# Optimization experiments

Measured on AMD Instinct MI355X. Metric: run time of the kernel, lower is better.

## Reference

```python
import jax, jax.numpy as jnp
import numpy as np

GROUP_SIZE = 128
HIDDEN = 2048
INTER = 5632
TOKENS = 8192
_SHIFTS = jnp.arange(8, dtype=jnp.uint32) * 4  # 4-bit nibbles, 8 per int32


def _pack_rows(nib):
    # nib: [in, out] int values in [0,16); pack 8 consecutive rows into one int32
    r, c = nib.shape
    n = nib.reshape(r // 8, 8, c).astype(jnp.uint32)
    packed = jnp.sum(n << _SHIFTS[None, :, None], axis=1, dtype=jnp.uint32)
    return jax.lax.bitcast_convert_type(packed, jnp.int32)  # [in//8, out]


def _pack_cols(nib):
    # nib: [groups, out]; pack 8 consecutive cols into one int32
    g, o = nib.shape
    n = nib.reshape(g, o // 8, 8).astype(jnp.uint32)
    packed = jnp.sum(n << _SHIFTS[None, None, :], axis=-1, dtype=jnp.uint32)
    return jax.lax.bitcast_convert_type(packed, jnp.int32)  # [groups, out//8]


def _dequant(qweight, qzeros, scales, group_size=GROUP_SIZE):
    # GPTQ int4 dequant: w = (q - (z + 1)) * scale, per group of `group_size` input rows
    in_packed, out = qweight.shape
    in_dim = in_packed * 8
    groups = scales.shape[0]
    sh = jnp.arange(8, dtype=jnp.int32) * 4
    q = (qweight[:, None, :] >> sh[None, :, None]) & 0xF       # [in//8, 8, out]
    q = q.reshape(in_dim, out)
    z = (qzeros[:, :, None] >> sh[None, None, :]) & 0xF        # [groups, out//8, 8]
    z = z.reshape(groups, out)
    gidx = jnp.arange(in_dim) // group_size                    # [in]
    w = (q - (z[gidx] + 1)).astype(scales.dtype) * scales[gidx]
    return w  # [in, out]


def setup_inputs() -> dict:
    key = jax.random.key(0)
    ks = jax.random.split(key, 10)
    x = jax.random.normal(ks[0], (TOKENS, HIDDEN), dtype=jnp.float32)

    def make(kq, kz, ksc, in_dim, out_dim):
        qn = jax.random.randint(kq, (in_dim, out_dim), 0, 16, dtype=jnp.int32)
        zn = jax.random.randint(kz, (in_dim // GROUP_SIZE, out_dim), 0, 16, dtype=jnp.int32)
        sc = jax.random.uniform(ksc, (in_dim // GROUP_SIZE, out_dim), jnp.float32, 1e-3, 2e-2)
        return _pack_rows(qn), _pack_cols(zn), sc

    gq, gz, gs = make(ks[1], ks[2], ks[3], HIDDEN, INTER)
    uq, uz, us = make(ks[4], ks[5], ks[6], HIDDEN, INTER)
    dq, dz, ds = make(ks[7], ks[8], ks[9], INTER, HIDDEN)
    return {
        "x": x,
        "gate_qweight": gq, "gate_qzeros": gz, "gate_scales": gs,
        "up_qweight": uq, "up_qzeros": uz, "up_scales": us,
        "down_qweight": dq, "down_qzeros": dz, "down_scales": ds,
    }


def reference(x, gate_qweight, gate_qzeros, gate_scales,
              up_qweight, up_qzeros, up_scales,
              down_qweight, down_qzeros, down_scales):
    wg = _dequant(gate_qweight, gate_qzeros, gate_scales)  # [H, I]
    wu = _dequant(up_qweight, up_qzeros, up_scales)        # [H, I]
    wd = _dequant(down_qweight, down_qzeros, down_scales)  # [I, H]
    # fused_gate_up: silu(x @ Wg) * (x @ Wu)
    h = jax.nn.silu(x @ wg) * (x @ wu)                     # [T, I]
    return h @ wd                                          # [T, H]
```

## Files before the change

### kernel.cpp

```cpp
#include <hip/hip_runtime.h>

#define TOKENS 8192
#define HIDDEN 2048
#define INTER  5632

typedef _Float16 f16x8 __attribute__((ext_vector_type(8)));
typedef float    f32x4 __attribute__((ext_vector_type(4)));

__device__ __forceinline__ void async_copy16(const void* g, void* l) {
  __builtin_amdgcn_global_load_lds(
      (const __attribute__((address_space(1))) unsigned int*)g,
      (__attribute__((address_space(3))) unsigned int*)l, 16, 0, 0);
}

#define BAR   __builtin_amdgcn_s_barrier()
#define SB0   __builtin_amdgcn_sched_barrier(0)
#define LGKM0 do { asm volatile("s_waitcnt lgkmcnt(0)" ::: "memory"); SB0; } while (0)
#define WAITVM(n) asm volatile("s_waitcnt vmcnt(" #n ")" ::: "memory")
#define PRIO(x) __builtin_amdgcn_s_setprio(x)


__global__ __launch_bounds__(256)
void k_convert_x(const float* __restrict__ x, _Float16* __restrict__ xs) {
  __shared__ float lt[64 * 33];
  const int kb0  = blockIdx.x;
  const int mt32 = blockIdx.y;
  const int t    = threadIdx.x;

  const int m_l  = t >> 3;
  const int k4a  = t & 7;
  const float* row = x + (size_t)(mt32 * 32 + m_l) * HIDDEN + kb0 * 64;
#pragma unroll
  for (int h = 0; h < 2; ++h) {
    const int k4 = k4a + h * 8;
    const float4 f = *(const float4*)(row + k4 * 4);
    lt[(k4 * 4 + 0) * 33 + m_l] = f.x;
    lt[(k4 * 4 + 1) * 33 + m_l] = f.y;
    lt[(k4 * 4 + 2) * 33 + m_l] = f.z;
    lt[(k4 * 4 + 3) * 33 + m_l] = f.w;
  }
  __syncthreads();

  const int kb_l = t >> 5;
  const int m_o  = t & 31;
  f16x8 v;
#pragma unroll
  for (int j = 0; j < 8; ++j)
    v[j] = (_Float16)lt[(kb_l * 8 + j) * 33 + m_o];
  const int kb   = kb0 * 8 + kb_l;
  const int mt128 = mt32 >> 2;
  const int m128  = (mt32 & 3) * 32 + m_o;
  *(f16x8*)(xs + ((size_t)(mt128 * 256 + kb) * 128 + m128) * 8) = v;
}

__global__ void k_dequant(const unsigned int* __restrict__ qw,
                          const unsigned int* __restrict__ qz,
                          const float* __restrict__ sc,
                          _Float16* __restrict__ out, int N, int N8) {
  const int n  = blockIdx.x * 256 + threadIdx.x;
  const int k8 = blockIdx.y;
  const int g  = k8 >> 4;
  unsigned int q  = qw[(size_t)k8 * N + n];
  unsigned int zw = qz[(size_t)g * N8 + (n >> 3)];
  int   z1 = (int)((zw >> ((n & 7) * 4)) & 0xFu) + 1;
  float s  = sc[(size_t)g * N + n];
  f16x8 w;
#pragma unroll
  for (int j = 0; j < 8; ++j)
    w[j] = (_Float16)((float)((int)((q >> (4 * j)) & 0xFu) - z1) * s);
  *(f16x8*)(out + ((size_t)k8 * N + n) * 8) = w;
}

__global__ __launch_bounds__(256, 2)
void k_gemm_gateup(const _Float16* __restrict__ xs,
                   const _Float16* __restrict__ wg,
                   const _Float16* __restrict__ wu,
                   _Float16* __restrict__ hs) {
  __shared__ _Float16 lds[3 * 8192];
  _Float16* Al  = lds;
  _Float16* Bgl = lds + 8192;
  _Float16* Bul = lds + 16384;
  const int nt = blockIdx.x, mt = blockIdx.y;
  const int tid = threadIdx.x;
  const int wave = tid >> 6, lane = tid & 63;
  const int wm = wave >> 1, wn = wave & 1;
  const int row16 = lane >> 4, col = lane & 15;
  const int slot = wave * 4;

  const _Float16* gA = xs + (size_t)mt * 256 * 1024;

  int afo[4], bfo[4];
#pragma unroll
  for (int i = 0; i < 4; ++i) {
    afo[i] = (row16 * 128 + wm * 64 + i * 16 + col) * 8;
    bfo[i] = (row16 * 128 + wn * 64 + i * 16 + col) * 8;
  }

  const f32x4 zero = {0.f, 0.f, 0.f, 0.f};
  f32x4 accg[4][4], accu[4][4];
#pragma unroll
  for (int i = 0; i < 4; ++i)
#pragma unroll
    for (int j = 0; j < 4; ++j) { accg[i][j] = zero; accu[i][j] = zero; }

  for (int kit = 0; kit < HIDDEN / 64; ++kit) {
    __syncthreads();
#pragma unroll
    for (int q = 0; q < 4; ++q) {
      const int c = (slot + q) * 64 + lane;
      async_copy16(gA + (size_t)kit * 8192 + (size_t)c * 8,
                   (char*)Al + (size_t)(slot + q) * 1024);
      const int kbl = c >> 7, cc = c & 127;
      const size_t bo = ((size_t)(kit * 8 + kbl) * INTER + nt * 128 + cc) * 8;
      async_copy16(wg + bo, (char*)Bgl + (size_t)(slot + q) * 1024);
      async_copy16(wu + bo, (char*)Bul + (size_t)(slot + q) * 1024);
    }
    __syncthreads();
#pragma unroll
    for (int ks = 0; ks < 2; ++ks) {
      const int kadd = ks * 4096;
      f16x8 af[4], bg[4], bu[4];
#pragma unroll
      for (int i = 0; i < 4; ++i) {
        af[i] = *(const f16x8*)(Al  + kadd + afo[i]);
        bg[i] = *(const f16x8*)(Bgl + kadd + bfo[i]);
        bu[i] = *(const f16x8*)(Bul + kadd + bfo[i]);
      }
#pragma unroll
      for (int mi = 0; mi < 4; ++mi)
#pragma unroll
        for (int ni = 0; ni < 4; ++ni) {
          accg[mi][ni] = __builtin_amdgcn_mfma_f32_16x16x32_f16(af[mi], bg[ni], accg[mi][ni], 0, 0, 0);
          accu[mi][ni] = __builtin_amdgcn_mfma_f32_16x16x32_f16(af[mi], bu[ni], accu[mi][ni], 0, 0, 0);
        }
    }
  }
#pragma unroll
  for (int mi = 0; mi < 4; ++mi)
#pragma unroll
    for (int ni = 0; ni < 4; ++ni) {
      const int kg = nt * 128 + wn * 64 + ni * 16 + col;
      const size_t base = (size_t)(mt * (INTER / 8) + (kg >> 3)) * 1024 + (kg & 7);
#pragma unroll
      for (int r = 0; r < 4; ++r) {
        float g = accg[mi][ni][r], u = accu[mi][ni][r];
        float h = g / (1.f + __expf(-g)) * u;
        const int ml = wm * 64 + mi * 16 + row16 * 4 + r;
        hs[base + (size_t)ml * 8] = (_Float16)h;
      }
    }
}

__global__ __launch_bounds__(512, 1)
void k_gemm_down(const _Float16* __restrict__ hs,
                 const _Float16* __restrict__ wd,
                 float* __restrict__ out) {
  extern __shared__ _Float16 lds[];
  _Float16* A0 = lds;
  _Float16* A1 = lds + 16384;
  _Float16* B0 = lds + 32768;
  _Float16* B1 = lds + 49152;

  const int bid  = blockIdx.x;
  const int wgid = (bid & 7) * 32 + (bid >> 3);
  const int nt = wgid >> 5, mt = wgid & 31;

  const int tid  = threadIdx.x;
  const int wave = tid >> 6, lane = tid & 63;
  const int wm = wave >> 2, wn = wave & 3;
  const int row16 = lane >> 4, col = lane & 15;

  int afo[8], bfo[4];
#pragma unroll
  for (int i = 0; i < 8; ++i)
    afo[i] = wm * 8192 + row16 * 1024 + (i * 16 + col) * 8;
#pragma unroll
  for (int i = 0; i < 4; ++i)
    bfo[i] = row16 * 2048 + (wn * 64 + i * 16 + col) * 8;

  const f32x4 zero = {0.f, 0.f, 0.f, 0.f};
  f32x4 acc[8][4];
#pragma unroll
  for (int i = 0; i < 8; ++i)
#pragma unroll
    for (int j = 0; j < 4; ++j) acc[i][j] = zero;

  f16x8 af[4][2], bf[4][2];

#define DN_LOAD_A(AP, mh) \
  _Pragma("unroll") for (int mi_ = 0; mi_ < 4; ++mi_) \
  _Pragma("unroll") for (int ks_ = 0; ks_ < 2; ++ks_) \
    af[mi_][ks_] = *(const f16x8*)((AP) + afo[(mh) * 4 + mi_] + ks_ * 4096);

#define DN_LOAD_B(BP, nh) \
  _Pragma("unroll") for (int ni_ = 0; ni_ < 2; ++ni_) \
  _Pragma("unroll") for (int ks_ = 0; ks_ < 2; ++ks_) \
    bf[(nh) * 2 + ni_][ks_] = *(const f16x8*)((BP) + bfo[(nh) * 2 + ni_] + ks_ * 8192);

#define DN_MFMA(mh, nh) \
  _Pragma("unroll") for (int mi_ = 0; mi_ < 4; ++mi_) \
  _Pragma("unroll") for (int ni_ = 0; ni_ < 2; ++ni_) \
  _Pragma("unroll") for (int ks_ = 0; ks_ < 2; ++ks_) \
    acc[(mh) * 4 + mi_][(nh) * 2 + ni_] = __builtin_amdgcn_mfma_f32_16x16x32_f16( \
        af[mi_][ks_], bf[(nh) * 2 + ni_][ks_], acc[(mh) * 4 + mi_][(nh) * 2 + ni_], 0, 0, 0);

#define DN_STAGE_A(AP, kt) do { const int kt_ = (kt); \
  _Pragma("unroll") for (int q_ = 0; q_ < 4; ++q_) { \
    const int i_ = q_ * 512 + tid; \
    async_copy16(hs + (size_t)(((2 * mt + (i_ >> 10)) * 704 + kt_ * 8 + ((i_ >> 7) & 7)) * 128 + (i_ & 127)) * 8, \
                 (char*)(AP) + q_ * 8192 + wave * 1024); } } while (0)

#define DN_STAGE_B(BP, kt) do { const int kt_ = (kt); \
  _Pragma("unroll") for (int q_ = 0; q_ < 4; ++q_) { \
    const int i_ = q_ * 512 + tid; \
    async_copy16(wd + (size_t)((kt_ * 8 + (i_ >> 8)) * HIDDEN + nt * 256 + (i_ & 255)) * 8, \
                 (char*)(BP) + q_ * 8192 + wave * 1024); } } while (0)

  DN_STAGE_B(B0, 0); DN_STAGE_A(A0, 0);
  DN_STAGE_B(B1, 1); DN_STAGE_A(A1, 1);
  WAITVM(8);
  BAR; SB0;

  for (int t2 = 0; t2 < 44; ++t2) {
    const int e2 = (2 * t2 + 2 < 88) ? 2 * t2 + 2 : 87;
    const int o2 = (2 * t2 + 3 < 88) ? 2 * t2 + 3 : 87;
    DN_LOAD_A(A0, 0); DN_LOAD_B(B0, 0);
    BAR; LGKM0; PRIO(1); DN_MFMA(0, 0); PRIO(0); BAR; SB0;
    DN_LOAD_B(B0, 1);
    BAR; LGKM0; PRIO(1); DN_MFMA(0, 1); PRIO(0); BAR; SB0;
    DN_LOAD_A(A0, 1); DN_STAGE_B(B0, e2);
    BAR; LGKM0; PRIO(1); DN_MFMA(1, 0); PRIO(0); BAR; SB0;
    DN_STAGE_A(A0, e2);
    BAR; LGKM0; PRIO(1); DN_MFMA(1, 1); PRIO(0); WAITVM(8); BAR; SB0;
    DN_LOAD_A(A1, 0); DN_LOAD_B(B1, 0);
    BAR; LGKM0; PRIO(1); DN_MFMA(0, 0); PRIO(0); BAR; SB0;
    DN_LOAD_B(B1, 1);
    BAR; LGKM0; PRIO(1); DN_MFMA(0, 1); PRIO(0); BAR; SB0;
    DN_LOAD_A(A1, 1); DN_STAGE_B(B1, o2);
    BAR; LGKM0; PRIO(1); DN_MFMA(1, 0); PRIO(0); BAR; SB0;
    DN_STAGE_A(A1, o2);
    BAR; LGKM0; PRIO(1); DN_MFMA(1, 1); PRIO(0); WAITVM(8); BAR; SB0;
  }
  WAITVM(0);

#pragma unroll
  for (int mi = 0; mi < 8; ++mi)
#pragma unroll
    for (int ni = 0; ni < 4; ++ni) {
      const int n = nt * 256 + wn * 64 + ni * 16 + col;
#pragma unroll
      for (int r = 0; r < 4; ++r) {
        const int m = mt * 256 + wm * 128 + mi * 16 + row16 * 4 + r;
        out[(size_t)m * HIDDEN + n] = acc[mi][ni][r];
      }
    }
#undef DN_LOAD_A
#undef DN_LOAD_B
#undef DN_MFMA
#undef DN_STAGE_A
#undef DN_STAGE_B
}

extern "C" void kernel_launch(void* const* d_in, const int* in_sizes, int n_in,
                              void* d_out, int out_size, void* d_ws, size_t ws_size,
                              hipStream_t stream) {
  (void)in_sizes; (void)n_in; (void)out_size; (void)ws_size;
  const float*        x  = (const float*)d_in[0];
  const unsigned int* gq = (const unsigned int*)d_in[1];
  const unsigned int* gz = (const unsigned int*)d_in[2];
  const float*        gs = (const float*)d_in[3];
  const unsigned int* uq = (const unsigned int*)d_in[4];
  const unsigned int* uz = (const unsigned int*)d_in[5];
  const float*        us = (const float*)d_in[6];
  const unsigned int* dq = (const unsigned int*)d_in[7];
  const unsigned int* dz = (const unsigned int*)d_in[8];
  const float*        ds = (const float*)d_in[9];
  float* out = (float*)d_out;

  char* ws = (char*)d_ws;
  _Float16* xs  = (_Float16*)ws;
  _Float16* wgd = (_Float16*)(ws + (size_t)TOKENS * HIDDEN * 2);
  _Float16* wud = wgd + (size_t)HIDDEN * INTER;
  _Float16* wdd = wud + (size_t)HIDDEN * INTER;
  _Float16* hs  = wdd + (size_t)INTER * HIDDEN;

  static bool attr_set = false;
  if (!attr_set) {
    hipFuncSetAttribute((const void*)k_gemm_down,
                        hipFuncAttributeMaxDynamicSharedMemorySize, 131072);
    attr_set = true;
  }

  k_convert_x<<<dim3(HIDDEN / 64, TOKENS / 32), 256, 0, stream>>>(x, xs);
  k_dequant<<<dim3(INTER / 256, HIDDEN / 8), 256, 0, stream>>>(gq, gz, gs, wgd, INTER, INTER / 8);
  k_dequant<<<dim3(INTER / 256, HIDDEN / 8), 256, 0, stream>>>(uq, uz, us, wud, INTER, INTER / 8);
  k_dequant<<<dim3(HIDDEN / 256, INTER / 8), 256, 0, stream>>>(dq, dz, ds, wdd, HIDDEN, HIDDEN / 8);
  k_gemm_gateup<<<dim3(INTER / 128, TOKENS / 128), 256, 0, stream>>>(xs, wgd, wud, hs);
  k_gemm_down<<<dim3(256), 512, 131072, stream>>>(hs, wdd, out);
}
```

Before: 661.3 us.

## Fuse int4 gate/up dequantization into gate-up GEMM using fp16 magic-number trick

Removes the two separate dequant kernels for the gate and up weights. The gate-up GEMM now loads packed int4 words straight from global memory into registers and dequantizes them in-register with the 0x6400 fp16 bias trick and packed half2 subtract/multiply. The x conversion permutes the K order within each group of 8 to match the interleaved nibble layout. This cuts the fp16 weight write and read traffic and two launches, but it adds ALU work and un-staged global loads inside the MFMA loop, and scales are rounded to fp16.

```diff
diff --git a/kernel.cpp b/kernel.cpp
--- a/kernel.cpp
+++ b/kernel.cpp
@@ -5,6 +5,7 @@
 #define INTER  5632
 
 typedef _Float16 f16x8 __attribute__((ext_vector_type(8)));
+typedef _Float16 f16x2 __attribute__((ext_vector_type(2)));
 typedef float    f32x4 __attribute__((ext_vector_type(4)));
 
 __device__ __forceinline__ void async_copy16(const void* g, void* l) {
@@ -18,6 +19,18 @@
 #define LGKM0 do { asm volatile("s_waitcnt lgkmcnt(0)" ::: "memory"); SB0; } while (0)
 #define WAITVM(n) asm volatile("s_waitcnt vmcnt(" #n ")" ::: "memory")
 #define PRIO(x) __builtin_amdgcn_s_setprio(x)
+
+__device__ __forceinline__ f16x8 dq8(unsigned int q, f16x2 s2, f16x2 c2) {
+  union { unsigned int u[4]; f16x8 v; } r;
+#pragma unroll
+  for (int j = 0; j < 4; ++j) {
+    const unsigned int t = ((q >> (4 * j)) & 0x000F000Fu) | 0x64006400u;
+    f16x2 h = __builtin_bit_cast(f16x2, t);
+    h = (h - c2) * s2;
+    r.u[j] = __builtin_bit_cast(unsigned int, h);
+  }
+  return r.v;
+}
 
 
 __global__ __launch_bounds__(256)
@@ -43,10 +56,11 @@
 
   const int kb_l = t >> 5;
   const int m_o  = t & 31;
+  const int P[8] = {0, 4, 1, 5, 2, 6, 3, 7};
   f16x8 v;
 #pragma unroll
   for (int j = 0; j < 8; ++j)
-    v[j] = (_Float16)lt[(kb_l * 8 + j) * 33 + m_o];
+    v[j] = (_Float16)lt[(kb_l * 8 + P[j]) * 33 + m_o];
   const int kb   = kb0 * 8 + kb_l;
   const int mt128 = mt32 >> 2;
   const int m128  = (mt32 & 3) * 32 + m_o;
@@ -73,13 +87,14 @@
 
 __global__ __launch_bounds__(256, 2)
 void k_gemm_gateup(const _Float16* __restrict__ xs,
-                   const _Float16* __restrict__ wg,
-                   const _Float16* __restrict__ wu,
+                   const unsigned int* __restrict__ gq,
+                   const unsigned int* __restrict__ gz,
+                   const float* __restrict__ gs,
+                   const unsigned int* __restrict__ uq,
+                   const unsigned int* __restrict__ uz,
+                   const float* __restrict__ us,
                    _Float16* __restrict__ hs) {
-  __shared__ _Float16 lds[3 * 8192];
-  _Float16* Al  = lds;
-  _Float16* Bgl = lds + 8192;
-  _Float16* Bul = lds + 16384;
+  __shared__ _Float16 Al[8192];
   const int nt = blockIdx.x, mt = blockIdx.y;
   const int tid = threadIdx.x;
   const int wave = tid >> 6, lane = tid & 63;
@@ -89,11 +104,11 @@
 
   const _Float16* gA = xs + (size_t)mt * 256 * 1024;
 
-  int afo[4], bfo[4];
+  int afo[4], ncol[4];
 #pragma unroll
   for (int i = 0; i < 4; ++i) {
-    afo[i] = (row16 * 128 + wm * 64 + i * 16 + col) * 8;
-    bfo[i] = (row16 * 128 + wn * 64 + i * 16 + col) * 8;
+    afo[i]  = (row16 * 128 + wm * 64 + i * 16 + col) * 8;
+    ncol[i] = nt * 128 + wn * 64 + i * 16 + col;
   }
 
   const f32x4 zero = {0.f, 0.f, 0.f, 0.f};
@@ -103,28 +118,59 @@
 #pragma unroll
     for (int j = 0; j < 4; ++j) { accg[i][j] = zero; accu[i][j] = zero; }
 
+  f16x2 sg2[4], cg2[4], su2[4], cu2[4];
+
   for (int kit = 0; kit < HIDDEN / 64; ++kit) {
+    if ((kit & 1) == 0) {
+      const int g = kit >> 1;
+#pragma unroll
+      for (int ni = 0; ni < 4; ++ni) {
+        const int n = ncol[ni];
+        const float        sgf = gs[(size_t)g * INTER + n];
+        const float        suf = us[(size_t)g * INTER + n];
+        const unsigned int zgw = gz[(size_t)g * (INTER / 8) + (n >> 3)];
+        const unsigned int zuw = uz[(size_t)g * (INTER / 8) + (n >> 3)];
+        const int z1g = (int)((zgw >> ((n & 7) * 4)) & 0xFu) + 1;
+        const int z1u = (int)((zuw >> ((n & 7) * 4)) & 0xFu) + 1;
+        const _Float16 shg = (_Float16)sgf, shu = (_Float16)suf;
+        const _Float16 chg = (_Float16)(float)(1024 + z1g);
+        const _Float16 chu = (_Float16)(float)(1024 + z1u);
+        sg2[ni] = (f16x2){shg, shg}; cg2[ni] = (f16x2){chg, chg};
+        su2[ni] = (f16x2){shu, shu}; cu2[ni] = (f16x2){chu, chu};
+      }
+    }
+
+    unsigned int bqg[2][4], bqu[2][4];
+#pragma unroll
+    for (int ks = 0; ks < 2; ++ks) {
+      const size_t ro = (size_t)((kit * 8 + ks * 4 + row16)) * INTER;
+#pragma unroll
+      for (int ni = 0; ni < 4; ++ni) {
+        bqg[ks][ni] = gq[ro + ncol[ni]];
+        bqu[ks][ni] = uq[ro + ncol[ni]];
+      }
+    }
+
     __syncthreads();
 #pragma unroll
     for (int q = 0; q < 4; ++q) {
       const int c = (slot + q) * 64 + lane;
       async_copy16(gA + (size_t)kit * 8192 + (size_t)c * 8,
                    (char*)Al + (size_t)(slot + q) * 1024);
-      const int kbl = c >> 7, cc = c & 127;
-      const size_t bo = ((size_t)(kit * 8 + kbl) * INTER + nt * 128 + cc) * 8;
-      async_copy16(wg + bo, (char*)Bgl + (size_t)(slot + q) * 1024);
-      async_copy16(wu + bo, (char*)Bul + (size_t)(slot + q) * 1024);
     }
     __syncthreads();
+
 #pragma unroll
     for (int ks = 0; ks < 2; ++ks) {
       const int kadd = ks * 4096;
       f16x8 af[4], bg[4], bu[4];
 #pragma unroll
-      for (int i = 0; i < 4; ++i) {
-        af[i] = *(const f16x8*)(Al  + kadd + afo[i]);
-        bg[i] = *(const f16x8*)(Bgl + kadd + bfo[i]);
-        bu[i] = *(const f16x8*)(Bul + kadd + bfo[i]);
+      for (int i = 0; i < 4; ++i)
+        af[i] = *(const f16x8*)(Al + kadd + afo[i]);
+#pragma unroll
+      for (int ni = 0; ni < 4; ++ni) {
+        bg[ni] = dq8(bqg[ks][ni], sg2[ni], cg2[ni]);
+        bu[ni] = dq8(bqu[ks][ni], su2[ni], cu2[ni]);
       }
 #pragma unroll
       for (int mi = 0; mi < 4; ++mi)
@@ -139,7 +185,7 @@
   for (int mi = 0; mi < 4; ++mi)
 #pragma unroll
     for (int ni = 0; ni < 4; ++ni) {
-      const int kg = nt * 128 + wn * 64 + ni * 16 + col;
+      const int kg = ncol[ni];
       const size_t base = (size_t)(mt * (INTER / 8) + (kg >> 3)) * 1024 + (kg & 7);
 #pragma unroll
       for (int r = 0; r < 4; ++r) {
@@ -279,9 +325,7 @@
 
   char* ws = (char*)d_ws;
   _Float16* xs  = (_Float16*)ws;
-  _Float16* wgd = (_Float16*)(ws + (size_t)TOKENS * HIDDEN * 2);
-  _Float16* wud = wgd + (size_t)HIDDEN * INTER;
-  _Float16* wdd = wud + (size_t)HIDDEN * INTER;
+  _Float16* wdd = (_Float16*)(ws + (size_t)TOKENS * HIDDEN * 2);
   _Float16* hs  = wdd + (size_t)INTER * HIDDEN;
 
   static bool attr_set = false;
@@ -292,9 +336,8 @@
   }
 
   k_convert_x<<<dim3(HIDDEN / 64, TOKENS / 32), 256, 0, stream>>>(x, xs);
-  k_dequant<<<dim3(INTER / 256, HIDDEN / 8), 256, 0, stream>>>(gq, gz, gs, wgd, INTER, INTER / 8);
-  k_dequant<<<dim3(INTER / 256, HIDDEN / 8), 256, 0, stream>>>(uq, uz, us, wud, INTER, INTER / 8);
   k_dequant<<<dim3(HIDDEN / 256, INTER / 8), 256, 0, stream>>>(dq, dz, ds, wdd, HIDDEN, HIDDEN / 8);
-  k_gemm_gateup<<<dim3(INTER / 128, TOKENS / 128), 256, 0, stream>>>(xs, wgd, wud, hs);
+  k_gemm_gateup<<<dim3(INTER / 128, TOKENS / 128), 256, 0, stream>>>(
+      xs, gq, gz, gs, uq, uz, us, hs);
   k_gemm_down<<<dim3(256), 512, 131072, stream>>>(hs, wdd, out);
 }
```

Measured after the change: 761.7 us. 15.2% more time.
